# Performance work log

Hardware: AMD Instinct MI355X
Metric: run time of the kernel (lower is better)

The kernel has to match this reference:

```python
import jax, jax.numpy as jnp
import numpy as np

B, T, I, H = 512, 2048, 13, 13


def setup_inputs() -> dict:
    key = jax.random.key(0)
    ks = jax.random.split(key, 7)
    s_in = 1.0 / np.sqrt(H)
    return {
        "x": jax.random.normal(ks[0], (B, T, I), dtype=jnp.float32),
        "W_ih": jax.random.uniform(ks[1], (4 * H, I), jnp.float32, -s_in, s_in),
        "W_hh": jax.random.uniform(ks[2], (4 * H, H), jnp.float32, -s_in, s_in),
        "b_ih": jax.random.uniform(ks[3], (4 * H,), jnp.float32, -s_in, s_in),
        "b_hh": jax.random.uniform(ks[4], (4 * H,), jnp.float32, -s_in, s_in),
        "fc_w": jax.random.uniform(ks[5], (1, H), jnp.float32, -s_in, s_in),
        "fc_b": jax.random.uniform(ks[6], (1,), jnp.float32, -s_in, s_in),
    }


def _lstm(x, W_ih, W_hh, b_ih, b_hh):
    # Precompute input-to-gate projections for all timesteps: [B, T, 4H]
    xg = jnp.einsum("bti,gi->btg", x, W_ih) + b_ih + b_hh
    xg = jnp.swapaxes(xg, 0, 1)  # [T, B, 4H] for scan
    h0 = jnp.zeros((x.shape[0], H), x.dtype)
    c0 = jnp.zeros((x.shape[0], H), x.dtype)

    def step(carry, xg_t):
        h, c = carry
        gates = xg_t + h @ W_hh.T  # [B, 4H]
        i_g, f_g, g_g, o_g = jnp.split(gates, 4, axis=-1)  # PyTorch order i,f,g,o
        i_g = jax.nn.sigmoid(i_g)
        f_g = jax.nn.sigmoid(f_g)
        g_g = jnp.tanh(g_g)
        o_g = jax.nn.sigmoid(o_g)
        c_new = f_g * c + i_g * g_g
        h_new = o_g * jnp.tanh(c_new)
        return (h_new, c_new), h_new

    _, hs = jax.lax.scan(step, (h0, c0), xg)  # hs: [T, B, H]
    return jnp.swapaxes(hs, 0, 1)  # [B, T, H]


def reference(x, W_ih, W_hh, b_ih, b_hh, fc_w, fc_b):
    out = _lstm(x, W_ih, W_hh, b_ih, b_hh)  # [B, T, H]
    out = jnp.einsum("bth,oh->bto", out, fc_w) + fc_b  # [B, T, 1]
    return jax.nn.sigmoid(out)
```

## Files before the change

kernel.cpp:

```cpp
#include <hip/hip_runtime.h>

#define BB 512
#define TT 2048

__device__ __forceinline__ float fexp2(float x){ return __builtin_amdgcn_exp2f(x); }
__device__ __forceinline__ float frcp(float x){ return __builtin_amdgcn_rcpf(x); }

#define QB(v, ctrl) __int_as_float(__builtin_amdgcn_mov_dpp(__float_as_int(v), (ctrl), 0xF, 0xF, true))
#define RL(v, l)    __builtin_amdgcn_readlane((v), (l))

__global__ __launch_bounds__(64, 1) void k_rec_f(
    const float* __restrict__ x,
    const float* __restrict__ Wih,
    const float* __restrict__ Whh,
    const float* __restrict__ bih,
    const float* __restrict__ bhh,
    const float* __restrict__ fcw,
    const float* __restrict__ fcb,
    float* __restrict__ out)
{
  const int lane = threadIdx.x;
  const int b    = blockIdx.x;
  const int q    = lane & 3;
  const int j    = lane >> 2;
  const int jc   = (j < 13) ? j : 12;
  const bool fcl = (lane == 52);
  const int e    = fcl ? 0 : q*13 + jc;

  const float kq = (q==2) ? -2.8853900817779268f : -1.4426950408889634f;
  const float gm = (q==2) ? -5.7707801635558536f : 1.f;
  const float ga = (q==2) ?  2.8853900817779268f : 0.f;
  const float fcbias = -1.4426950408889634f * fcb[0];

  const float* wsrc = fcl ? fcw : (Whh + e*13);
  const float  kx   = fcl ? 0.f : kq;

  float w[13], wx[13];
  #pragma unroll
  for (int k=0;k<13;k++) w[k]  = wsrc[k]*kq;
  #pragma unroll
  for (int k=0;k<13;k++) wx[k] = Wih[e*13+k]*kx;

  const float biass = fcl ? fcbias : (bih[e]+bhh[e])*kq;

  const float* xb = x + (size_t)b*(TT*13);
  const int ll = (lane < 52) ? lane : 51;

  float2 xcur = ((const float2*)(xb      ))[ll];
  float2 xnxt = ((const float2*)(xb + 104))[ll];

  float h = 0.f, c_ = 0.f;
  float hb0=0,hb1=0,hb2=0,hb3=0,hb4=0,hb5=0,hb6=0,hb7=0,hb8=0,hb9=0,hb10=0,hb11=0,hb12=0;

  float p0=0,p1=0,p2=0,p3=0,p4=0,p5=0,p6=0,p7=0;
  float* op = out + (size_t)b*TT;
  bool first = true;

#define CAPTURE(gv_, u_) do {                                                 \
    if ((u_)==1) p0=(gv_); else if ((u_)==2) p1=(gv_);                        \
    else if ((u_)==3) p2=(gv_); else if ((u_)==4) p3=(gv_);                   \
    else if ((u_)==5) p4=(gv_); else if ((u_)==6) p5=(gv_);                   \
    else if ((u_)==7) p6=(gv_);                                               \
    else { p7=(gv_);                                                          \
      if (!first){                                                            \
        if (lane == 52){                                                      \
          float4* o4 = (float4*)op;                                           \
          o4[0] = make_float4(p0,p1,p2,p3);                                   \
          o4[1] = make_float4(p4,p5,p6,p7);                                   \
        }                                                                     \
        op += 8;                                                              \
      }                                                                       \
      first = false;                                                          \
    }                                                                         \
  } while(0)

#define STEP(xv_, u_) do {                                                    \
    float dA = fmaf(w[0], hb0, (xv_));                                        \
    dA = fmaf(w[1], hb1, dA);                                                 \
    dA = fmaf(w[2], hb2, dA);                                                 \
    dA = fmaf(w[3], hb3, dA);                                                 \
    dA = fmaf(w[4], hb4, dA);                                                 \
    float dB = w[5]*hb5;                                                      \
    dB = fmaf(w[6], hb6, dB);                                                 \
    dB = fmaf(w[7], hb7, dB);                                                 \
    dB = fmaf(w[8], hb8, dB);                                                 \
    float dC = w[9]*hb9;                                                      \
    dC = fmaf(w[10], hb10, dC);                                               \
    dC = fmaf(w[11], hb11, dC);                                               \
    dC = fmaf(w[12], hb12, dC);                                               \
    float s  = (dB + dC) + dA;                                                \
    float r  = frcp(1.f + fexp2(s));                                          \
    float g  = fmaf(gm, r, ga);                                               \
    CAPTURE(g, u_);                                                           \
    float ggb = QB(g, 0xAA);                                                  \
    float gfb = QB(g, 0x55);                                                  \
    float gob = QB(g, 0xFF);                                                  \
    float go2 = gob + gob;                                                    \
    c_ = fmaf(gfb, c_, g*ggb);                                                \
    float r2 = frcp(1.f + fexp2(c_));                                         \
    h = fmaf(go2, r2, -gob);                                                  \
    int hv_ = __float_as_int(h);                                              \
    hb0  = __int_as_float(RL(hv_, 0));                                        \
    hb1  = __int_as_float(RL(hv_, 4));                                        \
    hb2  = __int_as_float(RL(hv_, 8));                                        \
    hb3  = __int_as_float(RL(hv_, 12));                                       \
    hb4  = __int_as_float(RL(hv_, 16));                                       \
    hb5  = __int_as_float(RL(hv_, 20));                                       \
    hb6  = __int_as_float(RL(hv_, 24));                                       \
    hb7  = __int_as_float(RL(hv_, 28));                                       \
    hb8  = __int_as_float(RL(hv_, 32));                                       \
    hb9  = __int_as_float(RL(hv_, 36));                                       \
    hb10 = __int_as_float(RL(hv_, 40));                                       \
    hb11 = __int_as_float(RL(hv_, 44));                                       \
    hb12 = __int_as_float(RL(hv_, 48));                                       \
  } while(0)

#define STEPX(u_) do {                                                        \
    float sx_ = biass;                                                        \
    _Pragma("unroll")                                                         \
    for (int k_ = 0; k_ < 13; ++k_){                                          \
      const int f_ = (u_)*13 + k_;                                            \
      float xe_ = (f_ & 1) ? xcur.y : xcur.x;                                 \
      sx_ = fmaf(wx[k_], __int_as_float(RL(__float_as_int(xe_), f_>>1)), sx_);\
    }                                                                         \
    STEP(sx_, u_);                                                            \
  } while(0)

  for (int g=0; g<256; ++g){
    const int gn = (g+2 < 256) ? (g+2) : 255;
    float2 xfut = ((const float2*)(xb + (size_t)gn*104))[ll];
    STEPX(0); STEPX(1); STEPX(2); STEPX(3);
    STEPX(4); STEPX(5); STEPX(6); STEPX(7);
    xcur = xnxt; xnxt = xfut;
  }

  {
    float s = fcbias;
    s = fmaf(w[0],  hb0,  s);
    s = fmaf(w[1],  hb1,  s);
    s = fmaf(w[2],  hb2,  s);
    s = fmaf(w[3],  hb3,  s);
    s = fmaf(w[4],  hb4,  s);
    s = fmaf(w[5],  hb5,  s);
    s = fmaf(w[6],  hb6,  s);
    s = fmaf(w[7],  hb7,  s);
    s = fmaf(w[8],  hb8,  s);
    s = fmaf(w[9],  hb9,  s);
    s = fmaf(w[10], hb10, s);
    s = fmaf(w[11], hb11, s);
    s = fmaf(w[12], hb12, s);
    float r = frcp(1.f + fexp2(s));
    if (lane == 52){
      float4* o4 = (float4*)op;
      o4[0] = make_float4(p0,p1,p2,p3);
      o4[1] = make_float4(p4,p5,p6,r);
    }
  }

#undef STEPX
#undef STEP
#undef CAPTURE
}

extern "C" void kernel_launch(void* const* d_in, const int* in_sizes, int n_in,
                              void* d_out, int out_size, void* d_ws, size_t ws_size,
                              hipStream_t stream)
{
  const float* x   = (const float*)d_in[0];
  const float* Wih = (const float*)d_in[1];
  const float* Whh = (const float*)d_in[2];
  const float* bih = (const float*)d_in[3];
  const float* bhh = (const float*)d_in[4];
  const float* fcw = (const float*)d_in[5];
  const float* fcb = (const float*)d_in[6];
  float* out = (float*)d_out;

  (void)d_ws; (void)ws_size;
  k_rec_f<<<dim3(BB), dim3(64), 0, stream>>>(x, Wih, Whh, bih, bhh, fcw, fcb, out);
}
```

Before: 380.9 us.

## Split input projection into a producer wave feeding the recurrence via LDS double buffer

Adds a second wavefront per block that computes the input-to-gate projections for 64-step chunks into a double-buffered shared-memory array, while the first wavefront runs only the recurrent step and reads the precomputed values from LDS. This takes the 13 readlane+FMA input projection per step off the serial critical path. In exchange it adds a block barrier every 64 steps, LDS reads on the recurrence path, and a second wave competing for the SIMD.

```diff
diff --git a/kernel.cpp b/kernel.cpp
--- a/kernel.cpp
+++ b/kernel.cpp
@@ -2,6 +2,8 @@
 
 #define BB 512
 #define TT 2048
+#define CH 64
+#define NCH (TT/CH)
 
 __device__ __forceinline__ float fexp2(float x){ return __builtin_amdgcn_exp2f(x); }
 __device__ __forceinline__ float frcp(float x){ return __builtin_amdgcn_rcpf(x); }
@@ -9,7 +11,7 @@
 #define QB(v, ctrl) __int_as_float(__builtin_amdgcn_mov_dpp(__float_as_int(v), (ctrl), 0xF, 0xF, true))
 #define RL(v, l)    __builtin_amdgcn_readlane((v), (l))
 
-__global__ __launch_bounds__(64, 1) void k_rec_f(
+__global__ __launch_bounds__(128, 1) void k_fused(
     const float* __restrict__ x,
     const float* __restrict__ Wih,
     const float* __restrict__ Whh,
@@ -19,42 +21,42 @@
     const float* __restrict__ fcb,
     float* __restrict__ out)
 {
-  const int lane = threadIdx.x;
+  __shared__ float sxbuf[2][CH][64];
+
+  const int tid  = threadIdx.x;
+  const int wid  = tid >> 6;
+  const int lane = tid & 63;
   const int b    = blockIdx.x;
-  const int q    = lane & 3;
-  const int j    = lane >> 2;
-  const int jc   = (j < 13) ? j : 12;
-  const bool fcl = (lane == 52);
-  const int e    = fcl ? 0 : q*13 + jc;
-
-  const float kq = (q==2) ? -2.8853900817779268f : -1.4426950408889634f;
-  const float gm = (q==2) ? -5.7707801635558536f : 1.f;
-  const float ga = (q==2) ?  2.8853900817779268f : 0.f;
-  const float fcbias = -1.4426950408889634f * fcb[0];
-
-  const float* wsrc = fcl ? fcw : (Whh + e*13);
-  const float  kx   = fcl ? 0.f : kq;
-
-  float w[13], wx[13];
-  #pragma unroll
-  for (int k=0;k<13;k++) w[k]  = wsrc[k]*kq;
-  #pragma unroll
-  for (int k=0;k<13;k++) wx[k] = Wih[e*13+k]*kx;
-
-  const float biass = fcl ? fcbias : (bih[e]+bhh[e])*kq;
-
-  const float* xb = x + (size_t)b*(TT*13);
-  const int ll = (lane < 52) ? lane : 51;
-
-  float2 xcur = ((const float2*)(xb      ))[ll];
-  float2 xnxt = ((const float2*)(xb + 104))[ll];
-
+  const float* xp = x + (size_t)b*(TT*13);
+
+  float wxp[13]; float biasp = 0.f;
+  float w[13];
+  float kgm = 1.f, kga = 0.f, fcbias = 0.f;
+  int   e = 0;
   float h = 0.f, c_ = 0.f;
   float hb0=0,hb1=0,hb2=0,hb3=0,hb4=0,hb5=0,hb6=0,hb7=0,hb8=0,hb9=0,hb10=0,hb11=0,hb12=0;
-
   float p0=0,p1=0,p2=0,p3=0,p4=0,p5=0,p6=0,p7=0;
   float* op = out + (size_t)b*TT;
   bool first = true;
+
+#define FILL(bi_, t0_) do {                                                   \
+    _Pragma("unroll 2")                                                       \
+    for (int tt=0; tt<CH; tt+=4){                                             \
+      const float* rp = xp + (size_t)((t0_)+tt)*13;                           \
+      float a0=biasp, a1=biasp, a2=biasp, a3=biasp;                           \
+      _Pragma("unroll")                                                       \
+      for (int k=0;k<13;++k){                                                 \
+        a0 = fmaf(wxp[k], rp[k],    a0);                                      \
+        a1 = fmaf(wxp[k], rp[13+k], a1);                                      \
+        a2 = fmaf(wxp[k], rp[26+k], a2);                                      \
+        a3 = fmaf(wxp[k], rp[39+k], a3);                                      \
+      }                                                                       \
+      sxbuf[bi_][tt+0][lane] = a0;                                            \
+      sxbuf[bi_][tt+1][lane] = a1;                                            \
+      sxbuf[bi_][tt+2][lane] = a2;                                            \
+      sxbuf[bi_][tt+3][lane] = a3;                                            \
+    }                                                                         \
+  } while(0)
 
 #define CAPTURE(gv_, u_) do {                                                 \
     if ((u_)==1) p0=(gv_); else if ((u_)==2) p1=(gv_);                        \
@@ -90,7 +92,7 @@
     dC = fmaf(w[12], hb12, dC);                                               \
     float s  = (dB + dC) + dA;                                                \
     float r  = frcp(1.f + fexp2(s));                                          \
-    float g  = fmaf(gm, r, ga);                                               \
+    float g  = fmaf(kgm, r, kga);                                             \
     CAPTURE(g, u_);                                                           \
     float ggb = QB(g, 0xAA);                                                  \
     float gfb = QB(g, 0x55);                                                  \
@@ -115,26 +117,58 @@
     hb12 = __int_as_float(RL(hv_, 48));                                       \
   } while(0)
 
-#define STEPX(u_) do {                                                        \
-    float sx_ = biass;                                                        \
+#define CONSUME(bi_) do {                                                     \
+    float rc[8], rn[8];                                                       \
     _Pragma("unroll")                                                         \
-    for (int k_ = 0; k_ < 13; ++k_){                                          \
-      const int f_ = (u_)*13 + k_;                                            \
-      float xe_ = (f_ & 1) ? xcur.y : xcur.x;                                 \
-      sx_ = fmaf(wx[k_], __int_as_float(RL(__float_as_int(xe_), f_>>1)), sx_);\
+    for (int u=0;u<8;++u) rc[u] = sxbuf[bi_][u][e];                           \
+    _Pragma("unroll 2")                                                       \
+    for (int g=0; g<CH/8; ++g){                                               \
+      const int tn = (g < CH/8-1) ? ((g+1)<<3) : 0;  \
+      _Pragma("unroll")                                                       \
+      for (int u=0;u<8;++u) rn[u] = sxbuf[bi_][tn+u][e];                      \
+      STEP(rc[0],0); STEP(rc[1],1); STEP(rc[2],2); STEP(rc[3],3);             \
+      STEP(rc[4],4); STEP(rc[5],5); STEP(rc[6],6); STEP(rc[7],7);             \
+      _Pragma("unroll")                                                       \
+      for (int u=0;u<8;++u) rc[u] = rn[u];                                    \
     }                                                                         \
-    STEP(sx_, u_);                                                            \
-  } while(0)
-
-  for (int g=0; g<256; ++g){
-    const int gn = (g+2 < 256) ? (g+2) : 255;
-    float2 xfut = ((const float2*)(xb + (size_t)gn*104))[ll];
-    STEPX(0); STEPX(1); STEPX(2); STEPX(3);
-    STEPX(4); STEPX(5); STEPX(6); STEPX(7);
-    xcur = xnxt; xnxt = xfut;
+  } while(0)
+
+  if (wid == 1){
+    const int  l     = lane;
+    const bool fcrow = (l == 52);
+    const int  row   = (l < 52) ? l : 0;
+    const float kql  = (l >= 26 && l < 39) ? -2.8853900817779268f : -1.4426950408889634f;
+    const float kx   = fcrow ? 0.f : kql;
+    #pragma unroll
+    for (int k=0;k<13;k++) wxp[k] = Wih[row*13+k]*kx;
+    biasp = fcrow ? (-1.4426950408889634f * fcb[0])
+                  : ((l < 52) ? (bih[row]+bhh[row])*kql : 0.f);
+    FILL(0, 0);
+  } else {
+    const int  q   = lane & 3;
+    const int  j   = lane >> 2;
+    const int  jc  = (j < 13) ? j : 12;
+    const bool fcl = (lane == 52);
+    e = fcl ? 52 : q*13 + jc;
+    const float kq = (q==2) ? -2.8853900817779268f : -1.4426950408889634f;
+    kgm = (q==2) ? -5.7707801635558536f : 1.f;
+    kga = (q==2) ?  2.8853900817779268f : 0.f;
+    fcbias = -1.4426950408889634f * fcb[0];
+    const float* wsrc = fcl ? fcw : (Whh + (size_t)e*13);
+    #pragma unroll
+    for (int k=0;k<13;k++) w[k] = wsrc[k]*kq;
   }
-
-  {
+  __syncthreads();
+
+  for (int c=0; c<NCH-1; ++c){
+    if (wid == 1){ FILL((c+1)&1, (c+1)*CH); }
+    else         { CONSUME(c&1); }
+    __syncthreads();
+  }
+
+  if (wid == 0){
+    CONSUME((NCH-1)&1);
+
     float s = fcbias;
     s = fmaf(w[0],  hb0,  s);
     s = fmaf(w[1],  hb1,  s);
@@ -157,9 +191,10 @@
     }
   }
 
-#undef STEPX
+#undef CONSUME
 #undef STEP
 #undef CAPTURE
+#undef FILL
 }
 
 extern "C" void kernel_launch(void* const* d_in, const int* in_sizes, int n_in,
@@ -176,5 +211,5 @@
   float* out = (float*)d_out;
 
   (void)d_ws; (void)ws_size;
-  k_rec_f<<<dim3(BB), dim3(64), 0, stream>>>(x, Wih, Whh, bih, bhh, fcw, fcb, out);
+  k_fused<<<dim3(BB), dim3(128), 0, stream>>>(x, Wih, Whh, bih, bhh, fcw, fcb, out);
 }
```

Measured after the change: 365.4 us. -4.1%, faster.

## Offload input projection to producer wave via double-buffered fp16 LDS

Applied to the files above, without the earlier changes.

Adds a second wavefront that computes the input-to-gate projections for 64 timesteps at a time and stores them as fp16 in double-buffered shared memory. The recurrent wave then reads precomputed gate inputs with vector LDS loads instead of doing 13 readlane+FMA per step on the critical path. This moves the x-projection off the serial recurrence chain, at the cost of block-wide barriers every 64 steps and fp16 rounding of the gate preactivations, which may affect accuracy.

```diff
diff --git a/kernel.cpp b/kernel.cpp
--- a/kernel.cpp
+++ b/kernel.cpp
@@ -1,15 +1,18 @@
 #include <hip/hip_runtime.h>
+#include <hip/hip_fp16.h>
 
 #define BB 512
 #define TT 2048
 
+typedef _Float16 half2v __attribute__((ext_vector_type(2)));
+
 __device__ __forceinline__ float fexp2(float x){ return __builtin_amdgcn_exp2f(x); }
 __device__ __forceinline__ float frcp(float x){ return __builtin_amdgcn_rcpf(x); }
 
 #define QB(v, ctrl) __int_as_float(__builtin_amdgcn_mov_dpp(__float_as_int(v), (ctrl), 0xF, 0xF, true))
 #define RL(v, l)    __builtin_amdgcn_readlane((v), (l))
 
-__global__ __launch_bounds__(64, 1) void k_rec_f(
+__global__ __launch_bounds__(128, 1) void k_pc(
     const float* __restrict__ x,
     const float* __restrict__ Wih,
     const float* __restrict__ Whh,
@@ -19,42 +22,46 @@
     const float* __restrict__ fcb,
     float* __restrict__ out)
 {
-  const int lane = threadIdx.x;
+  __shared__ unsigned short xgb[2][8][424];
+
+  const int tid  = threadIdx.x;
+  const int wid  = tid >> 6;
+  const int lane = tid & 63;
   const int b    = blockIdx.x;
-  const int q    = lane & 3;
-  const int j    = lane >> 2;
-  const int jc   = (j < 13) ? j : 12;
-  const bool fcl = (lane == 52);
-  const int e    = fcl ? 0 : q*13 + jc;
-
-  const float kq = (q==2) ? -2.8853900817779268f : -1.4426950408889634f;
-  const float gm = (q==2) ? -5.7707801635558536f : 1.f;
-  const float ga = (q==2) ?  2.8853900817779268f : 0.f;
-  const float fcbias = -1.4426950408889634f * fcb[0];
-
-  const float* wsrc = fcl ? fcw : (Whh + e*13);
-  const float  kx   = fcl ? 0.f : kq;
-
-  float w[13], wx[13];
-  #pragma unroll
-  for (int k=0;k<13;k++) w[k]  = wsrc[k]*kq;
-  #pragma unroll
-  for (int k=0;k<13;k++) wx[k] = Wih[e*13+k]*kx;
-
-  const float biass = fcl ? fcbias : (bih[e]+bhh[e])*kq;
-
-  const float* xb = x + (size_t)b*(TT*13);
-  const int ll = (lane < 52) ? lane : 51;
-
-  float2 xcur = ((const float2*)(xb      ))[ll];
-  float2 xnxt = ((const float2*)(xb + 104))[ll];
-
+
+  float xr[13];
+  const int  tgl = lane >> 3, u = lane & 7;
+  const float* xbase = x + ((size_t)b*TT + tgl*8 + u)*13;
+  unsigned short fc16 = 0;
+
+  float w[13];
+  float gm = 1.f, ga = 0.f, fcbias = 0.f;
+  int   e = 0;
   float h = 0.f, c_ = 0.f;
   float hb0=0,hb1=0,hb2=0,hb3=0,hb4=0,hb5=0,hb6=0,hb7=0,hb8=0,hb9=0,hb10=0,hb11=0,hb12=0;
-
   float p0=0,p1=0,p2=0,p3=0,p4=0,p5=0,p6=0,p7=0;
   float* op = out + (size_t)b*TT;
   bool first = true;
+
+#define XLOAD(c_) do {                                                        \
+    const float* p_ = xbase + (size_t)(c_)*64*13;                             \
+    _Pragma("unroll")                                                         \
+    for (int k=0;k<13;++k) xr[k] = p_[k];                                     \
+  } while(0)
+
+#define FILL(bi_) do {                                                        \
+    unsigned short* dst_ = &xgb[bi_][tgl][0];                                 \
+    _Pragma("unroll 4")                                                       \
+    for (int g=0; g<52; ++g){                                                 \
+      float acc = bih[g] + bhh[g];                                            \
+      _Pragma("unroll")                                                       \
+      for (int k=0;k<13;++k) acc = fmaf(Wih[g*13+k], xr[k], acc);             \
+      const float sc = (g>=26 && g<39) ? -2.8853900817779268f                 \
+                                       : -1.4426950408889634f;                \
+      dst_[g*8 + u] = __half_as_ushort(__float2half(acc*sc));                 \
+    }                                                                         \
+    dst_[52*8 + u] = fc16;                                                    \
+  } while(0)
 
 #define CAPTURE(gv_, u_) do {                                                 \
     if ((u_)==1) p0=(gv_); else if ((u_)==2) p1=(gv_);                        \
@@ -115,26 +122,63 @@
     hb12 = __int_as_float(RL(hv_, 48));                                       \
   } while(0)
 
-#define STEPX(u_) do {                                                        \
-    float sx_ = biass;                                                        \
-    _Pragma("unroll")                                                         \
-    for (int k_ = 0; k_ < 13; ++k_){                                          \
-      const int f_ = (u_)*13 + k_;                                            \
-      float xe_ = (f_ & 1) ? xcur.y : xcur.x;                                 \
-      sx_ = fmaf(wx[k_], __int_as_float(RL(__float_as_int(xe_), f_>>1)), sx_);\
-    }                                                                         \
-    STEP(sx_, u_);                                                            \
-  } while(0)
-
-  for (int g=0; g<256; ++g){
-    const int gn = (g+2 < 256) ? (g+2) : 255;
-    float2 xfut = ((const float2*)(xb + (size_t)gn*104))[ll];
-    STEPX(0); STEPX(1); STEPX(2); STEPX(3);
-    STEPX(4); STEPX(5); STEPX(6); STEPX(7);
-    xcur = xnxt; xnxt = xfut;
+#define XLO(w_) (float)(__builtin_bit_cast(half2v, (w_)).x)
+#define XHI(w_) (float)(__builtin_bit_cast(half2v, (w_)).y)
+
+#define STEP8(Q) do {                                                         \
+    STEP(XLO(Q.x), 0); STEP(XHI(Q.x), 1);                                     \
+    STEP(XLO(Q.y), 2); STEP(XHI(Q.y), 3);                                     \
+    STEP(XLO(Q.z), 4); STEP(XHI(Q.z), 5);                                     \
+    STEP(XLO(Q.w), 6); STEP(XHI(Q.w), 7);                                     \
+  } while(0)
+
+#define CONSUME(bi_) do {                                                     \
+    const char* base_ = (const char*)&xgb[bi_][0][0] + (size_t)e*16;          \
+    uint4 r0 = *(const uint4*)(base_ + 0*848);                                \
+    uint4 r1 = *(const uint4*)(base_ + 1*848);                                \
+    uint4 r2 = *(const uint4*)(base_ + 2*848);                                \
+    uint4 r3 = *(const uint4*)(base_ + 3*848);                                \
+    uint4 r4 = *(const uint4*)(base_ + 4*848);                                \
+    uint4 r5 = *(const uint4*)(base_ + 5*848);                                \
+    uint4 r6 = *(const uint4*)(base_ + 6*848);                                \
+    uint4 r7 = *(const uint4*)(base_ + 7*848);                                \
+    STEP8(r0); STEP8(r1); STEP8(r2); STEP8(r3);                               \
+    STEP8(r4); STEP8(r5); STEP8(r6); STEP8(r7);                               \
+  } while(0)
+
+  if (wid == 1){
+    fc16 = __half_as_ushort(__float2half(-1.4426950408889634f * fcb[0]));
+    XLOAD(0);
+    FILL(0);
+    XLOAD(1);
+  } else {
+    const int q  = lane & 3;
+    const int j  = lane >> 2;
+    const int jc = (j < 13) ? j : 12;
+    e = (lane == 52) ? 52 : q*13 + jc;
+    const float kq = (q==2) ? -2.8853900817779268f : -1.4426950408889634f;
+    gm = (q==2) ? -5.7707801635558536f : 1.f;
+    ga = (q==2) ?  2.8853900817779268f : 0.f;
+    fcbias = -1.4426950408889634f * fcb[0];
+    const float* wsrc = (lane == 52) ? fcw : (Whh + (size_t)e*13);
+    #pragma unroll
+    for (int k=0;k<13;k++) w[k] = wsrc[k]*kq;
   }
-
-  {
+  __syncthreads();
+
+  for (int c=0; c<31; ++c){
+    if (wid == 1){
+      FILL((c+1)&1);
+      if (c < 30) XLOAD(c+2);
+    } else {
+      CONSUME(c&1);
+    }
+    __syncthreads();
+  }
+
+  if (wid == 0){
+    CONSUME(31&1);
+
     float s = fcbias;
     s = fmaf(w[0],  hb0,  s);
     s = fmaf(w[1],  hb1,  s);
@@ -157,9 +201,14 @@
     }
   }
 
-#undef STEPX
+#undef CONSUME
+#undef STEP8
 #undef STEP
 #undef CAPTURE
+#undef FILL
+#undef XLOAD
+#undef XLO
+#undef XHI
 }
 
 extern "C" void kernel_launch(void* const* d_in, const int* in_sizes, int n_in,
@@ -176,5 +225,5 @@
   float* out = (float*)d_out;
 
   (void)d_ws; (void)ws_size;
-  k_rec_f<<<dim3(BB), dim3(64), 0, stream>>>(x, Wih, Whh, bih, bhh, fcw, fcb, out);
+  k_pc<<<dim3(BB), dim3(128), 0, stream>>>(x, Wih, Whh, bih, bhh, fcw, fcb, out);
 }
```

Measured after the change: 307.8 us, median of 3. -19.2%, faster.

## Software-pipeline the input projection one group ahead of the recurrence

Applied to the files above, without the earlier changes.

The input-to-gate projection for the next group of 8 timesteps is now computed inside each recurrent step, interleaved after the gate DPP broadcasts, and stored in a second buffer that is swapped in each iteration. Previously each step computed its own projection right before the dependent recurrent dot product. The aim is to fill latency slots on the serial h→h chain with independent readlane and FMA work. The x tile is now loaded as two scalar loads per lane instead of one float2, and register pressure rises from the extra sxA/sxB buffers.

```diff
diff --git a/kernel.cpp b/kernel.cpp
--- a/kernel.cpp
+++ b/kernel.cpp
@@ -9,7 +9,7 @@
 #define QB(v, ctrl) __int_as_float(__builtin_amdgcn_mov_dpp(__float_as_int(v), (ctrl), 0xF, 0xF, true))
 #define RL(v, l)    __builtin_amdgcn_readlane((v), (l))
 
-__global__ __launch_bounds__(64, 1) void k_rec_f(
+__global__ __launch_bounds__(64, 1) void k_sp(
     const float* __restrict__ x,
     const float* __restrict__ Wih,
     const float* __restrict__ Whh,
@@ -25,36 +25,38 @@
   const int j    = lane >> 2;
   const int jc   = (j < 13) ? j : 12;
   const bool fcl = (lane == 52);
-  const int e    = fcl ? 0 : q*13 + jc;
+  const int e    = fcl ? 52 : q*13 + jc;
+  const int er   = fcl ? 0  : q*13 + jc;
 
   const float kq = (q==2) ? -2.8853900817779268f : -1.4426950408889634f;
   const float gm = (q==2) ? -5.7707801635558536f : 1.f;
   const float ga = (q==2) ?  2.8853900817779268f : 0.f;
   const float fcbias = -1.4426950408889634f * fcb[0];
 
-  const float* wsrc = fcl ? fcw : (Whh + e*13);
-  const float  kx   = fcl ? 0.f : kq;
-
-  float w[13], wx[13];
+  const float* wsrc = fcl ? fcw : (Whh + (size_t)e*13);
+  float w[13];
   #pragma unroll
-  for (int k=0;k<13;k++) w[k]  = wsrc[k]*kq;
+  for (int k=0;k<13;k++) w[k] = wsrc[k]*kq;
+
+  const float kx = fcl ? 0.f : kq;
+  float sxw[13];
   #pragma unroll
-  for (int k=0;k<13;k++) wx[k] = Wih[e*13+k]*kx;
-
+  for (int k=0;k<13;k++) sxw[k] = Wih[er*13+k]*kx;
   const float biass = fcl ? fcbias : (bih[e]+bhh[e])*kq;
 
   const float* xb = x + (size_t)b*(TT*13);
-  const int ll = (lane < 52) ? lane : 51;
-
-  float2 xcur = ((const float2*)(xb      ))[ll];
-  float2 xnxt = ((const float2*)(xb + 104))[ll];
+  const int lane2 = (lane < 40) ? lane : 39;
 
   float h = 0.f, c_ = 0.f;
   float hb0=0,hb1=0,hb2=0,hb3=0,hb4=0,hb5=0,hb6=0,hb7=0,hb8=0,hb9=0,hb10=0,hb11=0,hb12=0;
-
   float p0=0,p1=0,p2=0,p3=0,p4=0,p5=0,p6=0,p7=0;
   float* op = out + (size_t)b*TT;
   bool first = true;
+
+  float sxA[8], sxB[8];
+  float xr0, xr1, xn0, xn1;
+
+#define RLX(f_) __int_as_float(RL(__float_as_int(((f_) < 64) ? xr0 : xr1), (f_) & 63))
 
 #define CAPTURE(gv_, u_) do {                                                 \
     if ((u_)==1) p0=(gv_); else if ((u_)==2) p1=(gv_);                        \
@@ -74,8 +76,8 @@
     }                                                                         \
   } while(0)
 
-#define STEP(xv_, u_) do {                                                    \
-    float dA = fmaf(w[0], hb0, (xv_));                                        \
+#define STEPU(u_) do {                                                        \
+    float dA = fmaf(w[0], hb0, sxA[u_]);                                      \
     dA = fmaf(w[1], hb1, dA);                                                 \
     dA = fmaf(w[2], hb2, dA);                                                 \
     dA = fmaf(w[3], hb3, dA);                                                 \
@@ -95,6 +97,19 @@
     float ggb = QB(g, 0xAA);                                                  \
     float gfb = QB(g, 0x55);                                                  \
     float gob = QB(g, 0xFF);                                                  \
+    float tx0  = RLX((u_)*13+0);                                              \
+    float tx1  = RLX((u_)*13+1);                                              \
+    float tx2  = RLX((u_)*13+2);                                              \
+    float tx3  = RLX((u_)*13+3);                                              \
+    float tx4  = RLX((u_)*13+4);                                              \
+    float tx5  = RLX((u_)*13+5);                                              \
+    float tx6  = RLX((u_)*13+6);                                              \
+    float tx7  = RLX((u_)*13+7);                                              \
+    float tx8  = RLX((u_)*13+8);                                              \
+    float tx9  = RLX((u_)*13+9);                                              \
+    float tx10 = RLX((u_)*13+10);                                             \
+    float tx11 = RLX((u_)*13+11);                                             \
+    float tx12 = RLX((u_)*13+12);                                             \
     float go2 = gob + gob;                                                    \
     c_ = fmaf(gfb, c_, g*ggb);                                                \
     float r2 = frcp(1.f + fexp2(c_));                                         \
@@ -113,25 +128,45 @@
     hb10 = __int_as_float(RL(hv_, 40));                                       \
     hb11 = __int_as_float(RL(hv_, 44));                                       \
     hb12 = __int_as_float(RL(hv_, 48));                                       \
+    float a_ = biass;                                                         \
+    a_ = fmaf(sxw[0],  tx0,  a_);                                             \
+    a_ = fmaf(sxw[1],  tx1,  a_);                                             \
+    a_ = fmaf(sxw[2],  tx2,  a_);                                             \
+    a_ = fmaf(sxw[3],  tx3,  a_);                                             \
+    a_ = fmaf(sxw[4],  tx4,  a_);                                             \
+    a_ = fmaf(sxw[5],  tx5,  a_);                                             \
+    a_ = fmaf(sxw[6],  tx6,  a_);                                             \
+    a_ = fmaf(sxw[7],  tx7,  a_);                                             \
+    a_ = fmaf(sxw[8],  tx8,  a_);                                             \
+    a_ = fmaf(sxw[9],  tx9,  a_);                                             \
+    a_ = fmaf(sxw[10], tx10, a_);                                             \
+    a_ = fmaf(sxw[11], tx11, a_);                                             \
+    a_ = fmaf(sxw[12], tx12, a_);                                             \
+    sxB[u_] = a_;                                                             \
   } while(0)
 
-#define STEPX(u_) do {                                                        \
-    float sx_ = biass;                                                        \
+#define SXINIT(u_) do {                                                       \
+    float a_ = biass;                                                         \
     _Pragma("unroll")                                                         \
-    for (int k_ = 0; k_ < 13; ++k_){                                          \
-      const int f_ = (u_)*13 + k_;                                            \
-      float xe_ = (f_ & 1) ? xcur.y : xcur.x;                                 \
-      sx_ = fmaf(wx[k_], __int_as_float(RL(__float_as_int(xe_), f_>>1)), sx_);\
-    }                                                                         \
-    STEP(sx_, u_);                                                            \
+    for (int k_=0;k_<13;++k_)                                                 \
+      a_ = fmaf(sxw[k_], RLX((u_)*13+k_), a_);                                \
+    sxA[u_] = a_;                                                             \
   } while(0)
 
-  for (int g=0; g<256; ++g){
-    const int gn = (g+2 < 256) ? (g+2) : 255;
-    float2 xfut = ((const float2*)(xb + (size_t)gn*104))[ll];
-    STEPX(0); STEPX(1); STEPX(2); STEPX(3);
-    STEPX(4); STEPX(5); STEPX(6); STEPX(7);
-    xcur = xnxt; xnxt = xfut;
+  xr0 = xb[lane];  xr1 = xb[64+lane2];
+  SXINIT(0); SXINIT(1); SXINIT(2); SXINIT(3);
+  SXINIT(4); SXINIT(5); SXINIT(6); SXINIT(7);
+  xr0 = xb[104+lane];  xr1 = xb[104+64+lane2];
+
+  for (int gi=0; gi<256; ++gi){
+    const int gp = (gi+2 < 256) ? (gi+2) : 255;
+    const float* rp = xb + (size_t)gp*104;
+    xn0 = rp[lane];  xn1 = rp[64+lane2];
+    STEPU(0); STEPU(1); STEPU(2); STEPU(3);
+    STEPU(4); STEPU(5); STEPU(6); STEPU(7);
+    #pragma unroll
+    for (int u=0;u<8;++u) sxA[u] = sxB[u];
+    xr0 = xn0;  xr1 = xn1;
   }
 
   {
@@ -157,9 +192,10 @@
     }
   }
 
-#undef STEPX
-#undef STEP
+#undef SXINIT
+#undef STEPU
 #undef CAPTURE
+#undef RLX
 }
 
 extern "C" void kernel_launch(void* const* d_in, const int* in_sizes, int n_in,
@@ -176,5 +212,5 @@
   float* out = (float*)d_out;
 
   (void)d_ws; (void)ws_size;
-  k_rec_f<<<dim3(BB), dim3(64), 0, stream>>>(x, Wih, Whh, bih, bhh, fcw, fcb, out);
+  k_sp<<<dim3(BB), dim3(64), 0, stream>>>(x, Wih, Whh, bih, bhh, fcw, fcb, out);
 }
```

Measured after the change: 377.3 us. About the same (-0.9%).
